# Performance work log

Measured on AMD Instinct MI355X. Metric: run time of the kernel, lower is better.

Reference implementation:

```python
import jax, jax.numpy as jnp
import numpy as np
from jax.ops import segment_sum, segment_max

N_NODES = 50000
N_EDGES = 800000
N_GRAPHS = 512


def setup_inputs() -> dict:
    key = jax.random.key(0)
    ks = jax.random.split(key, 12)
    s = 0.1
    x = jax.random.normal(ks[0], (N_NODES, 3), dtype=jnp.float32)
    edge_index = jax.random.randint(ks[1], (2, N_EDGES), 0, N_NODES, dtype=jnp.int64)
    batch = jnp.sort(jax.random.randint(ks[2], (N_NODES,), 0, N_GRAPHS, dtype=jnp.int64))
    # GATConv(3, 64, heads=4): W [3, 4*64], att [4,64] each
    W1 = jax.random.normal(ks[3], (3, 256), dtype=jnp.float32) * s
    att_src1 = jax.random.normal(ks[4], (4, 64), dtype=jnp.float32) * s
    att_dst1 = jax.random.normal(ks[5], (4, 64), dtype=jnp.float32) * s
    bias1 = jnp.zeros((256,), dtype=jnp.float32)
    # GATConv(256, 128, heads=1)
    W2 = jax.random.normal(ks[6], (256, 128), dtype=jnp.float32) * s
    att_src2 = jax.random.normal(ks[7], (1, 128), dtype=jnp.float32) * s
    att_dst2 = jax.random.normal(ks[8], (1, 128), dtype=jnp.float32) * s
    bias2 = jnp.zeros((128,), dtype=jnp.float32)
    # Linear(128, 2)
    fcW = jax.random.normal(ks[9], (128, 2), dtype=jnp.float32) * s
    fcb = jnp.zeros((2,), dtype=jnp.float32)
    return {"x": x, "edge_index": edge_index, "batch": batch,
            "W1": W1, "att_src1": att_src1, "att_dst1": att_dst1, "bias1": bias1,
            "W2": W2, "att_src2": att_src2, "att_dst2": att_dst2, "bias2": bias2,
            "fcW": fcW, "fcb": fcb}


def gat_conv(x, src, dst, W, att_src, att_dst, bias):
    """PyG-style GATConv (concat heads). src->dst messages, softmax over dst."""
    N = x.shape[0]
    H, C = att_src.shape
    h = (x @ W).reshape(N, H, C)                      # [N,H,C]
    a_src = jnp.einsum('nhc,hc->nh', h, att_src)      # [N,H]
    a_dst = jnp.einsum('nhc,hc->nh', h, att_dst)      # [N,H]
    e = jax.nn.leaky_relu(a_src[src] + a_dst[dst], 0.2)  # [E,H]
    # segment softmax over incoming edges of each dst node
    emax = segment_max(e, dst, num_segments=N)        # [N,H]
    ee = jnp.exp(e - emax[dst])
    denom = segment_sum(ee, dst, num_segments=N)      # [N,H]
    alpha = ee / (denom[dst] + 1e-16)                 # [E,H]
    out = segment_sum(alpha[:, :, None] * h[src], dst, num_segments=N)  # [N,H,C]
    return out.reshape(N, H * C) + bias


def reference(x, edge_index, batch, W1, att_src1, att_dst1, bias1,
              W2, att_src2, att_dst2, bias2, fcW, fcb):
    N = x.shape[0]
    loops = jnp.arange(N, dtype=edge_index.dtype)
    src = jnp.concatenate([edge_index[0], loops])     # add self-loops (PyG default)
    dst = jnp.concatenate([edge_index[1], loops])
    h = jax.nn.relu(gat_conv(x, src, dst, W1, att_src1, att_dst1, bias1))
    h = jax.nn.relu(gat_conv(h, src, dst, W2, att_src2, att_dst2, bias2))
    # global mean pool per graph
    sums = segment_sum(h, batch, num_segments=N_GRAPHS)                # [G,128]
    counts = segment_sum(jnp.ones((N, 1), h.dtype), batch, num_segments=N_GRAPHS)
    pooled = sums / jnp.maximum(counts, 1.0)
    return pooled @ fcW + fcb                          # [G,2]
```

## Files before the change

kernel.cpp:

```cpp
#include <hip/hip_runtime.h>
#include <hip/hip_bf16.h>

#define NN 50000
#define NE 800000
#define ET (NN + NE)
#define NG 512
#define NCHUNK 196
#define NROWPAD 50048
#define CAP 64

#define SCAT_BLKS 831
#define A1P_BLKS 196
#define W2B_BLKS 128
#define BND_BLKS 3
#define FRONT_GRID (SCAT_BLKS + A1P_BLKS + W2B_BLKS + BND_BLKS)

typedef __attribute__((ext_vector_type(8))) short bf16x8;
typedef __attribute__((ext_vector_type(4))) float f32x4;

static __device__ __forceinline__ float lrelu(float x) { return x > 0.f ? x : 0.2f * x; }

static __device__ __forceinline__ ushort f2b(float f) {
    __hip_bfloat16 b = __float2bfloat16(f);
    return *(ushort*)&b;
}
static __device__ __forceinline__ float b2f(ushort u) {
    union { unsigned int i; float f; } v; v.i = ((unsigned int)u) << 16; return v.f;
}

__global__ __launch_bounds__(256) void k_front(
        const int* __restrict__ ei, int* __restrict__ cnt, ushort* __restrict__ csr,
        const float* __restrict__ x, const float* __restrict__ W1,
        const float* __restrict__ attS1, const float* __restrict__ attD1,
        float* __restrict__ xa1, float* __restrict__ a1d,
        const float* __restrict__ W2, ushort* __restrict__ wtb,
        const int* __restrict__ batch, int* __restrict__ bounds) {
    __shared__ float wsd[24];
    int b = blockIdx.x, tid = threadIdx.x;
    if (b < SCAT_BLKS) {
        int t = b * 256 + tid;
        int base = t * 4;
        if (base >= ET) return;
        int4 sv, dv;
        if (base < NE) {
            sv = *(const int4*)(ei + base);
            dv = *(const int4*)(ei + NE + base);
        } else {
            int ls = base - NE;
            sv.x = ls; sv.y = ls + 1; sv.z = ls + 2; sv.w = ls + 3;
            dv = sv;
        }
        int p0 = atomicAdd(&cnt[dv.x], 1);
        int p1 = atomicAdd(&cnt[dv.y], 1);
        int p2 = atomicAdd(&cnt[dv.z], 1);
        int p3 = atomicAdd(&cnt[dv.w], 1);
        csr[dv.x * CAP + p0] = (ushort)sv.x;
        csr[dv.y * CAP + p1] = (ushort)sv.y;
        csr[dv.z * CAP + p2] = (ushort)sv.z;
        csr[dv.w * CAP + p3] = (ushort)sv.w;
    } else if (b < SCAT_BLKS + A1P_BLKS) {
        if (tid < 24) {
            int sel = tid / 12, r = tid % 12;
            int i = r >> 2, h = r & 3;
            const float* att = sel ? attD1 : attS1;
            float s = 0.f;
            for (int c = 0; c < 64; c++) s += W1[i * 256 + h * 64 + c] * att[h * 64 + c];
            wsd[tid] = s;
        }
        __syncthreads();
        int n = (b - SCAT_BLKS) * 256 + tid;
        if (n >= NN) return;
        float x0 = x[n * 3], x1 = x[n * 3 + 1], x2 = x[n * 3 + 2];
        float4 r0, r1, dd;
        r0.x = x0; r0.y = x1; r0.z = x2;
        r0.w = x0 * wsd[0] + x1 * wsd[4] + x2 * wsd[8];
        r1.x = x0 * wsd[1] + x1 * wsd[5] + x2 * wsd[9];
        r1.y = x0 * wsd[2] + x1 * wsd[6] + x2 * wsd[10];
        r1.z = x0 * wsd[3] + x1 * wsd[7] + x2 * wsd[11];
        r1.w = 0.f;
        dd.x = x0 * wsd[12] + x1 * wsd[16] + x2 * wsd[20];
        dd.y = x0 * wsd[13] + x1 * wsd[17] + x2 * wsd[21];
        dd.z = x0 * wsd[14] + x1 * wsd[18] + x2 * wsd[22];
        dd.w = x0 * wsd[15] + x1 * wsd[19] + x2 * wsd[23];
        *(float4*)(xa1 + n * 8) = r0;
        *(float4*)(xa1 + n * 8 + 4) = r1;
        *(float4*)(a1d + n * 4) = dd;
    } else if (b < SCAT_BLKS + A1P_BLKS + W2B_BLKS) {
        int i = (b - SCAT_BLKS - A1P_BLKS) * 256 + tid;
        int k = i >> 7, c = i & 127;
        wtb[c * 256 + k] = f2b(W2[i]);
    } else {
        int g = (b - SCAT_BLKS - A1P_BLKS - W2B_BLKS) * 256 + tid;
        if (g > NG) return;
        int lo = 0, hi = NN;
        while (lo < hi) { int mid = (lo + hi) >> 1; if (batch[mid] < g) lo = mid + 1; else hi = mid; }
        bounds[g] = lo;
    }
}

__global__ void k_l1_aggr2(const float* __restrict__ xa1, const float* __restrict__ a1d,
                           const int* __restrict__ cnt, const ushort* __restrict__ csr,
                           float* __restrict__ xb) {
    int n = blockIdx.x * 256 + threadIdx.x;
    if (n >= NN) return;
    float4 ad = *(const float4*)(a1d + n * 4);
    int dg = cnt[n];
    const ushort* cp = csr + n * CAP;
    float a[4][3], l[4];
#pragma unroll
    for (int h = 0; h < 4; h++) { a[h][0] = a[h][1] = a[h][2] = 0.f; l[h] = 0.f; }
    int j = 0;
    for (; j + 4 <= dg; j += 4) {
        ushort4 ss = *(const ushort4*)(cp + j);
        int s0 = ss.x, s1 = ss.y, s2 = ss.z, s3 = ss.w;
        float4 p00 = *(const float4*)(xa1 + s0 * 8), p01 = *(const float4*)(xa1 + s0 * 8 + 4);
        float4 p10 = *(const float4*)(xa1 + s1 * 8), p11 = *(const float4*)(xa1 + s1 * 8 + 4);
        float4 p20 = *(const float4*)(xa1 + s2 * 8), p21 = *(const float4*)(xa1 + s2 * 8 + 4);
        float4 p30 = *(const float4*)(xa1 + s3 * 8), p31 = *(const float4*)(xa1 + s3 * 8 + 4);
#pragma unroll
        for (int q = 0; q < 4; q++) {
            float4 ra = (q == 0) ? p00 : (q == 1) ? p10 : (q == 2) ? p20 : p30;
            float4 rb = (q == 0) ? p01 : (q == 1) ? p11 : (q == 2) ? p21 : p31;
            float e0 = __expf(lrelu(ra.w + ad.x));
            float e1 = __expf(lrelu(rb.x + ad.y));
            float e2 = __expf(lrelu(rb.y + ad.z));
            float e3 = __expf(lrelu(rb.z + ad.w));
            a[0][0] = fmaf(e0, ra.x, a[0][0]); a[0][1] = fmaf(e0, ra.y, a[0][1]); a[0][2] = fmaf(e0, ra.z, a[0][2]); l[0] += e0;
            a[1][0] = fmaf(e1, ra.x, a[1][0]); a[1][1] = fmaf(e1, ra.y, a[1][1]); a[1][2] = fmaf(e1, ra.z, a[1][2]); l[1] += e1;
            a[2][0] = fmaf(e2, ra.x, a[2][0]); a[2][1] = fmaf(e2, ra.y, a[2][1]); a[2][2] = fmaf(e2, ra.z, a[2][2]); l[2] += e2;
            a[3][0] = fmaf(e3, ra.x, a[3][0]); a[3][1] = fmaf(e3, ra.y, a[3][1]); a[3][2] = fmaf(e3, ra.z, a[3][2]); l[3] += e3;
        }
    }
    for (; j < dg; j++) {
        int s = cp[j];
        float4 ra = *(const float4*)(xa1 + s * 8);
        float4 rb = *(const float4*)(xa1 + s * 8 + 4);
        float e0 = __expf(lrelu(ra.w + ad.x));
        float e1 = __expf(lrelu(rb.x + ad.y));
        float e2 = __expf(lrelu(rb.y + ad.z));
        float e3 = __expf(lrelu(rb.z + ad.w));
        a[0][0] = fmaf(e0, ra.x, a[0][0]); a[0][1] = fmaf(e0, ra.y, a[0][1]); a[0][2] = fmaf(e0, ra.z, a[0][2]); l[0] += e0;
        a[1][0] = fmaf(e1, ra.x, a[1][0]); a[1][1] = fmaf(e1, ra.y, a[1][1]); a[1][2] = fmaf(e1, ra.z, a[1][2]); l[1] += e1;
        a[2][0] = fmaf(e2, ra.x, a[2][0]); a[2][1] = fmaf(e2, ra.y, a[2][1]); a[2][2] = fmaf(e2, ra.z, a[2][2]); l[2] += e2;
        a[3][0] = fmaf(e3, ra.x, a[3][0]); a[3][1] = fmaf(e3, ra.y, a[3][1]); a[3][2] = fmaf(e3, ra.z, a[3][2]); l[3] += e3;
    }
    float o[12];
#pragma unroll
    for (int h = 0; h < 4; h++) {
        float inv = 1.f / (l[h] + 1e-16f);
        o[h * 3 + 0] = a[h][0] * inv;
        o[h * 3 + 1] = a[h][1] * inv;
        o[h * 3 + 2] = a[h][2] * inv;
    }
    *(float4*)(xb + n * 12) = *(float4*)(o);
    *(float4*)(xb + n * 12 + 4) = *(float4*)(o + 4);
    *(float4*)(xb + n * 12 + 8) = *(float4*)(o + 8);
}

__global__ __launch_bounds__(64) void k_gemm_mfma(
        const float* __restrict__ xb, const float* __restrict__ W1g,
        const float* __restrict__ b1g, const ushort* __restrict__ wtb,
        const float* __restrict__ attS2, const float* __restrict__ attD2,
        ushort* __restrict__ h2b, float* __restrict__ a2s, float* __restrict__ a2d) {
    __shared__ float W1s[768];
    __shared__ float b1s[256];
    int lane = threadIdx.x;
    int R = blockIdx.x * 32;
    if (R >= NN) return;
    for (int q = lane; q < 768; q += 64) W1s[q] = W1g[q];
    for (int q = lane; q < 256; q += 64) b1s[q] = b1g[q];
    __syncthreads();
    int row16 = lane & 15, kg = lane >> 4;

    float xr[2][12];
#pragma unroll
    for (int t = 0; t < 2; t++) {
        int row = R + t * 16 + row16;
        if (row < NN) {
            *(float4*)(&xr[t][0]) = *(const float4*)(xb + row * 12);
            *(float4*)(&xr[t][4]) = *(const float4*)(xb + row * 12 + 4);
            *(float4*)(&xr[t][8]) = *(const float4*)(xb + row * 12 + 8);
        } else {
#pragma unroll
            for (int q = 0; q < 12; q++) xr[t][q] = 0.f;
        }
    }

    f32x4 acc[2][8];
#pragma unroll
    for (int t = 0; t < 2; t++)
#pragma unroll
        for (int ct = 0; ct < 8; ct++) acc[t][ct] = (f32x4){0.f, 0.f, 0.f, 0.f};

    const ushort* Bb = wtb + (size_t)row16 * 256 + kg * 8;
#pragma unroll
    for (int s = 0; s < 8; s++) {
        int head = s >> 1;
        int c0 = s * 32 + kg * 8;
        bf16x8 a0, a1;
#pragma unroll
        for (int jj = 0; jj < 8; jj++) {
            int c = c0 + jj;
            float w0 = W1s[c], w1 = W1s[256 + c], w2 = W1s[512 + c], bb = b1s[c];
            float v0 = fmaxf(fmaf(xr[0][head * 3], w0, fmaf(xr[0][head * 3 + 1], w1, fmaf(xr[0][head * 3 + 2], w2, bb))), 0.f);
            float v1 = fmaxf(fmaf(xr[1][head * 3], w0, fmaf(xr[1][head * 3 + 1], w1, fmaf(xr[1][head * 3 + 2], w2, bb))), 0.f);
            a0[jj] = (short)f2b(v0);
            a1[jj] = (short)f2b(v1);
        }
#pragma unroll
        for (int ct = 0; ct < 8; ct++) {
            bf16x8 bfr = *(const bf16x8*)(Bb + ct * 16 * 256 + s * 32);
            acc[0][ct] = __builtin_amdgcn_mfma_f32_16x16x32_bf16(a0, bfr, acc[0][ct], 0, 0, 0);
            acc[1][ct] = __builtin_amdgcn_mfma_f32_16x16x32_bf16(a1, bfr, acc[1][ct], 0, 0, 0);
        }
    }

    float s2v[8], d2v[8];
#pragma unroll
    for (int ct = 0; ct < 8; ct++) {
        s2v[ct] = attS2[ct * 16 + row16];
        d2v[ct] = attD2[ct * 16 + row16];
    }
#pragma unroll
    for (int tau = 0; tau < 2; tau++) {
#pragma unroll
        for (int q = 0; q < 4; q++) {
            int row = R + tau * 16 + kg * 4 + q;
            float ps = 0.f, pd = 0.f;
            if (row < NN) {
#pragma unroll
                for (int ct = 0; ct < 8; ct++) {
                    float v = acc[tau][ct][q];
                    h2b[(size_t)row * 128 + ct * 16 + row16] = f2b(v);
                    ps = fmaf(v, s2v[ct], ps);
                    pd = fmaf(v, d2v[ct], pd);
                }
            }
            for (int o = 1; o < 16; o <<= 1) {
                ps += __shfl_xor(ps, o, 64);
                pd += __shfl_xor(pd, o, 64);
            }
            if (row < NN && row16 == 0) { a2s[row] = ps; a2d[row] = pd; }
        }
    }
}

__global__ void k_l2_aggr(const ushort* __restrict__ h2u, const float* __restrict__ a2s,
                          const float* __restrict__ a2d, const int* __restrict__ cnt,
                          const ushort* __restrict__ csr, const float* __restrict__ b2,
                          float* __restrict__ out2) {
    int n = blockIdx.x, t = threadIdx.x;
    float adm = a2d[n];
    int dg = cnt[n];
    const ushort* cp = csr + n * CAP;
    float accx = 0.f, accy = 0.f, l = 0.f;
    int j = 0;
    for (; j + 8 <= dg; j += 8) {
        ushort4 sA = *(const ushort4*)(cp + j);
        ushort4 sB = *(const ushort4*)(cp + j + 4);
        int s0 = sA.x, s1 = sA.y, s2 = sA.z, s3 = sA.w;
        int s4 = sB.x, s5 = sB.y, s6 = sB.z, s7 = sB.w;
        float e0 = a2s[s0], e1 = a2s[s1], e2 = a2s[s2], e3 = a2s[s3];
        float e4 = a2s[s4], e5 = a2s[s5], e6 = a2s[s6], e7 = a2s[s7];
        ushort2 u0 = *(const ushort2*)(h2u + (size_t)s0 * 128 + t * 2);
        ushort2 u1 = *(const ushort2*)(h2u + (size_t)s1 * 128 + t * 2);
        ushort2 u2 = *(const ushort2*)(h2u + (size_t)s2 * 128 + t * 2);
        ushort2 u3 = *(const ushort2*)(h2u + (size_t)s3 * 128 + t * 2);
        ushort2 u4 = *(const ushort2*)(h2u + (size_t)s4 * 128 + t * 2);
        ushort2 u5 = *(const ushort2*)(h2u + (size_t)s5 * 128 + t * 2);
        ushort2 u6 = *(const ushort2*)(h2u + (size_t)s6 * 128 + t * 2);
        ushort2 u7 = *(const ushort2*)(h2u + (size_t)s7 * 128 + t * 2);
        float p0 = __expf(lrelu(e0 + adm)), p1 = __expf(lrelu(e1 + adm));
        float p2 = __expf(lrelu(e2 + adm)), p3 = __expf(lrelu(e3 + adm));
        float p4 = __expf(lrelu(e4 + adm)), p5 = __expf(lrelu(e5 + adm));
        float p6 = __expf(lrelu(e6 + adm)), p7 = __expf(lrelu(e7 + adm));
        accx = fmaf(p0, b2f(u0.x), fmaf(p1, b2f(u1.x), fmaf(p2, b2f(u2.x), fmaf(p3, b2f(u3.x), accx))));
        accx = fmaf(p4, b2f(u4.x), fmaf(p5, b2f(u5.x), fmaf(p6, b2f(u6.x), fmaf(p7, b2f(u7.x), accx))));
        accy = fmaf(p0, b2f(u0.y), fmaf(p1, b2f(u1.y), fmaf(p2, b2f(u2.y), fmaf(p3, b2f(u3.y), accy))));
        accy = fmaf(p4, b2f(u4.y), fmaf(p5, b2f(u5.y), fmaf(p6, b2f(u6.y), fmaf(p7, b2f(u7.y), accy))));
        l += (p0 + p1) + (p2 + p3) + (p4 + p5) + (p6 + p7);
    }
    for (; j < dg; j++) {
        int s = cp[j];
        float p = __expf(lrelu(a2s[s] + adm));
        ushort2 u = *(const ushort2*)(h2u + (size_t)s * 128 + t * 2);
        accx = fmaf(p, b2f(u.x), accx);
        accy = fmaf(p, b2f(u.y), accy);
        l += p;
    }
    float inv = 1.f / (l + 1e-16f);
    int c = t * 2;
    float2 o;
    o.x = fmaxf(accx * inv + b2[c], 0.f);
    o.y = fmaxf(accy * inv + b2[c + 1], 0.f);
    *(float2*)(out2 + n * 128 + c) = o;
}

__global__ void k_pool_fc(const float* __restrict__ out2, const int* __restrict__ bounds,
                          const float* __restrict__ fcW, const float* __restrict__ fcb,
                          float* __restrict__ out) {
    int g = blockIdx.x, t = threadIdx.x;
    int s = bounds[g], e = bounds[g + 1];
    float s0 = 0.f, s1 = 0.f, s2 = 0.f, s3 = 0.f;
    int n = s;
    for (; n + 4 <= e; n += 4) {
        s0 += out2[n * 128 + t];
        s1 += out2[(n + 1) * 128 + t];
        s2 += out2[(n + 2) * 128 + t];
        s3 += out2[(n + 3) * 128 + t];
    }
    for (; n < e; n++) s0 += out2[n * 128 + t];
    float sum = (s0 + s1) + (s2 + s3);
    float cnt = (float)(e - s);
    float pooled = sum / fmaxf(cnt, 1.f);
    float p0 = pooled * fcW[t * 2 + 0];
    float p1 = pooled * fcW[t * 2 + 1];
    for (int o = 32; o; o >>= 1) {
        p0 += __shfl_down(p0, o, 64);
        p1 += __shfl_down(p1, o, 64);
    }
    __shared__ float l0[2], l1[2];
    if ((t & 63) == 0) { l0[t >> 6] = p0; l1[t >> 6] = p1; }
    __syncthreads();
    if (t == 0) {
        out[g * 2 + 0] = l0[0] + l0[1] + fcb[0];
        out[g * 2 + 1] = l1[0] + l1[1] + fcb[1];
    }
}

extern "C" void kernel_launch(void* const* d_in, const int* in_sizes, int n_in,
                              void* d_out, int out_size, void* d_ws, size_t ws_size,
                              hipStream_t stream) {
    (void)in_sizes; (void)n_in; (void)out_size; (void)ws_size;
    const float* x     = (const float*)d_in[0];
    const int*   ei    = (const int*)d_in[1];
    const int*   batch = (const int*)d_in[2];
    const float* W1    = (const float*)d_in[3];
    const float* attS1 = (const float*)d_in[4];
    const float* attD1 = (const float*)d_in[5];
    const float* b1    = (const float*)d_in[6];
    const float* W2    = (const float*)d_in[7];
    const float* attS2 = (const float*)d_in[8];
    const float* attD2 = (const float*)d_in[9];
    const float* b2    = (const float*)d_in[10];
    const float* fcW   = (const float*)d_in[11];
    const float* fcb   = (const float*)d_in[12];
    float* out = (float*)d_out;

    char* ws = (char*)d_ws;
    size_t off = 0;
    auto alloc = [&](size_t bytes) -> char* {
        char* p = ws + off;
        off = (off + bytes + 255) & ~(size_t)255;
        return p;
    };
    float*  xa1  = (float*)alloc((size_t)NN * 8 * 4);
    float*  a1d  = (float*)alloc((size_t)NN * 4 * 4);
    float*  xb   = (float*)alloc((size_t)NN * 12 * 4);
    int*    cnt  = (int*)alloc((size_t)NN * 4);
    ushort* csr  = (ushort*)alloc((size_t)NN * CAP * 2);
    ushort* wtb  = (ushort*)alloc((size_t)128 * 256 * 2);
    ushort* h2b  = (ushort*)alloc((size_t)NN * 128 * 2);
    float*  a2s  = (float*)alloc((size_t)NN * 4);
    float*  a2d  = (float*)alloc((size_t)NN * 4);
    int*    bounds = (int*)alloc((size_t)(NG + 1) * 4);
    float*  out2 = (float*)alloc((size_t)NN * 128 * 4);

    hipMemsetAsync(cnt, 0, (size_t)NN * 4, stream);
    k_front<<<FRONT_GRID, 256, 0, stream>>>(ei, cnt, csr, x, W1, attS1, attD1,
                                            xa1, a1d, W2, wtb, batch, bounds);
    k_l1_aggr2<<<NCHUNK, 256, 0, stream>>>(xa1, a1d, cnt, csr, xb);
    k_gemm_mfma<<<(NROWPAD / 32), 64, 0, stream>>>(xb, W1, b1, wtb, attS2, attD2, h2b, a2s, a2d);
    k_l2_aggr<<<NN, 64, 0, stream>>>(h2b, a2s, a2d, cnt, csr, b2, out2);
    k_pool_fc<<<NG, 128, 0, stream>>>(out2, bounds, fcW, fcb, out);
}
```

Before: 148.9 us.

## Build CSR via two-pass bucketed scatter with shared-memory atomics

Edge scattering into per-node CSR slots now goes through buckets of 64 destination nodes. The first pass does one global atomic per edge on a bucket counter, and the counters are padded to separate cache lines. A new kernel then places the edges into per-node slots using shared-memory atomics, with the goal of cutting contended global atomics and scattered 2-byte stores. The cost is an extra kernel launch and an extra write and read of a 3.4 MB intermediate buffer. BCAP is fixed at 1536 and the code does not check for bucket overflow.

```diff
diff --git a/kernel.cpp b/kernel.cpp
--- a/kernel.cpp
+++ b/kernel.cpp
@@ -9,6 +9,10 @@
 #define NROWPAD 50048
 #define CAP 64
 
+#define NBUK 782
+#define BCAP 1536
+#define BSTRIDE 16
+
 #define SCAT_BLKS 831
 #define A1P_BLKS 196
 #define W2B_BLKS 128
@@ -29,7 +33,7 @@
 }
 
 __global__ __launch_bounds__(256) void k_front(
-        const int* __restrict__ ei, int* __restrict__ cnt, ushort* __restrict__ csr,
+        const int* __restrict__ ei, int* __restrict__ bcnt, unsigned int* __restrict__ bstore,
         const float* __restrict__ x, const float* __restrict__ W1,
         const float* __restrict__ attS1, const float* __restrict__ attD1,
         float* __restrict__ xa1, float* __restrict__ a1d,
@@ -50,14 +54,15 @@
             sv.x = ls; sv.y = ls + 1; sv.z = ls + 2; sv.w = ls + 3;
             dv = sv;
         }
-        int p0 = atomicAdd(&cnt[dv.x], 1);
-        int p1 = atomicAdd(&cnt[dv.y], 1);
-        int p2 = atomicAdd(&cnt[dv.z], 1);
-        int p3 = atomicAdd(&cnt[dv.w], 1);
-        csr[dv.x * CAP + p0] = (ushort)sv.x;
-        csr[dv.y * CAP + p1] = (ushort)sv.y;
-        csr[dv.z * CAP + p2] = (ushort)sv.z;
-        csr[dv.w * CAP + p3] = (ushort)sv.w;
+        int b0 = dv.x >> 6, b1 = dv.y >> 6, b2 = dv.z >> 6, b3 = dv.w >> 6;
+        int p0 = atomicAdd(&bcnt[b0 * BSTRIDE], 1);
+        int p1 = atomicAdd(&bcnt[b1 * BSTRIDE], 1);
+        int p2 = atomicAdd(&bcnt[b2 * BSTRIDE], 1);
+        int p3 = atomicAdd(&bcnt[b3 * BSTRIDE], 1);
+        bstore[b0 * BCAP + p0] = ((unsigned int)sv.x << 6) | (unsigned int)(dv.x & 63);
+        bstore[b1 * BCAP + p1] = ((unsigned int)sv.y << 6) | (unsigned int)(dv.y & 63);
+        bstore[b2 * BCAP + p2] = ((unsigned int)sv.z << 6) | (unsigned int)(dv.z & 63);
+        bstore[b3 * BCAP + p3] = ((unsigned int)sv.w << 6) | (unsigned int)(dv.w & 63);
     } else if (b < SCAT_BLKS + A1P_BLKS) {
         if (tid < 24) {
             int sel = tid / 12, r = tid % 12;
@@ -95,6 +100,29 @@
         int lo = 0, hi = NN;
         while (lo < hi) { int mid = (lo + hi) >> 1; if (batch[mid] < g) lo = mid + 1; else hi = mid; }
         bounds[g] = lo;
+    }
+}
+
+__global__ __launch_bounds__(256) void k_csr(const int* __restrict__ bcnt,
+                                             const unsigned int* __restrict__ bstore,
+                                             ushort* __restrict__ csr, int* __restrict__ cnt) {
+    __shared__ int cur[64];
+    int b = blockIdx.x, tid = threadIdx.x;
+    if (tid < 64) cur[tid] = 0;
+    __syncthreads();
+    int nb = bcnt[b * BSTRIDE];
+    const unsigned int* bp = bstore + (size_t)b * BCAP;
+    for (int i = tid; i < nb; i += 256) {
+        unsigned int r = bp[i];
+        int dlow = r & 63;
+        int src = r >> 6;
+        int pos = atomicAdd(&cur[dlow], 1);
+        csr[(((size_t)b << 6) + dlow) * CAP + pos] = (ushort)src;
+    }
+    __syncthreads();
+    if (tid < 64) {
+        int node = (b << 6) + tid;
+        if (node < NN) cnt[node] = cur[tid];
     }
 }
 
@@ -359,6 +387,8 @@
     float*  xb   = (float*)alloc((size_t)NN * 12 * 4);
     int*    cnt  = (int*)alloc((size_t)NN * 4);
     ushort* csr  = (ushort*)alloc((size_t)NN * CAP * 2);
+    int*    bcnt = (int*)alloc((size_t)NBUK * BSTRIDE * 4);
+    unsigned int* bstore = (unsigned int*)alloc((size_t)NBUK * BCAP * 4);
     ushort* wtb  = (ushort*)alloc((size_t)128 * 256 * 2);
     ushort* h2b  = (ushort*)alloc((size_t)NN * 128 * 2);
     float*  a2s  = (float*)alloc((size_t)NN * 4);
@@ -366,9 +396,10 @@
     int*    bounds = (int*)alloc((size_t)(NG + 1) * 4);
     float*  out2 = (float*)alloc((size_t)NN * 128 * 4);
 
-    hipMemsetAsync(cnt, 0, (size_t)NN * 4, stream);
-    k_front<<<FRONT_GRID, 256, 0, stream>>>(ei, cnt, csr, x, W1, attS1, attD1,
+    hipMemsetAsync(bcnt, 0, (size_t)NBUK * BSTRIDE * 4, stream);
+    k_front<<<FRONT_GRID, 256, 0, stream>>>(ei, bcnt, bstore, x, W1, attS1, attD1,
                                             xa1, a1d, W2, wtb, batch, bounds);
+    k_csr<<<NBUK, 256, 0, stream>>>(bcnt, bstore, csr, cnt);
     k_l1_aggr2<<<NCHUNK, 256, 0, stream>>>(xa1, a1d, cnt, csr, xb);
     k_gemm_mfma<<<(NROWPAD / 32), 64, 0, stream>>>(xb, W1, b1, wtb, attS2, attD2, h2b, a2s, a2d);
     k_l2_aggr<<<NN, 64, 0, stream>>>(h2b, a2s, a2d, cnt, csr, b2, out2);
```

Result: slower. 154.9 us (+4.0%).
